# Kernel optimization log

Hardware: AMD Instinct MI355X
Metric: run time of the kernel (lower is better)

The kernel has to match this reference:

```python
import jax, jax.numpy as jnp
import numpy as np

N_NODES = 200_000
N_EDGES = 400_000
EMB_DIM = 128
HID_DIM = 24
N_TYPES = 8


def setup_inputs() -> dict:
    key = jax.random.key(0)
    k_emb, k_src, k_typ, k_w1, k_w2 = jax.random.split(key, 5)
    rgcn_emb = jax.random.normal(k_emb, (N_NODES, EMB_DIM), dtype=jnp.float32)
    edge_index = jax.random.randint(k_src, (2, N_EDGES), 0, N_NODES, dtype=jnp.int32)
    edge_type = jax.random.randint(k_typ, (N_EDGES,), 0, N_TYPES, dtype=jnp.int32)
    # per-edge-type 2-layer MLP params: Linear(2D->H), Linear(H->1)
    W1 = jax.random.normal(k_w1, (N_TYPES, 2 * EMB_DIM, HID_DIM), dtype=jnp.float32) * 0.05
    b1 = jnp.zeros((N_TYPES, HID_DIM), dtype=jnp.float32)
    W2 = jax.random.normal(k_w2, (N_TYPES, HID_DIM), dtype=jnp.float32) * 0.05
    b2 = jnp.zeros((N_TYPES,), dtype=jnp.float32)
    return {"rgcn_emb": rgcn_emb, "edge_index": edge_index, "edge_type": edge_type,
            "W1": W1, "b1": b1, "W2": W2, "b2": b2}


def reference(rgcn_emb, edge_index, edge_type, W1, b1, W2, b2):
    src, dst = edge_index[0], edge_index[1]
    # gather + concat: [E, 2D]
    edge_emb = jnp.concatenate([rgcn_emb[src], rgcn_emb[dst]], axis=-1)
    # dense per-type expert compute, then select by routing (MoE-style)
    h = jnp.einsum('ed,tdh->teh', edge_emb, W1) + b1[:, None, :]  # [T,E,H]
    h = jnp.where(h > 0, h, 0.01 * h)  # LeakyReLU(0.01)
    s = jnp.einsum('teh,th->te', h, W2) + b2[:, None]  # [T,E]
    onehot = jax.nn.one_hot(edge_type, N_TYPES, dtype=s.dtype)  # [E,T]
    scores = jnp.einsum('te,et->e', s, onehot)  # scatter-select per edge
    return (scores, rgcn_emb)
```

## Files before the change

### kernel.cpp

```cpp
#include <hip/hip_runtime.h>


typedef _Float16 h2 __attribute__((ext_vector_type(2)));
typedef float    f4 __attribute__((ext_vector_type(4)));

constexpr int N_NODES = 200000;
constexpr int N_EDGES = 400000;
constexpr int EMB_DIM = 128;
constexpr int HID     = 24;
constexpr int N_TYPES = 8;
constexpr int BLK     = 256;

constexpr int CHUNKS  = 128;
constexpr int CH_SZ   = N_EDGES / CHUNKS;
constexpr int MAX_PAD = N_EDGES + N_TYPES * (BLK - 1);
constexpr int SCORE_BLOCKS = (MAX_PAD + BLK - 1) / BLK;
constexpr int COPY_BLOCKS  = 1024;

constexpr int PREP_HIST = CHUNKS;
constexpr int PREP_W1   = 16;
constexpr int PREP_CONV = 1024;
constexpr int PREP_BLOCKS = PREP_HIST + PREP_W1 + PREP_CONV;

constexpr int OFF_CC     = 0;
constexpr int OFF_COUNTS = OFF_CC + CHUNKS * N_TYPES;
constexpr int OFF_POFF   = OFF_COUNTS + N_TYPES;
constexpr int OFF_SORTED = OFF_POFF + N_TYPES;
constexpr size_t SORT_BYTES  = (size_t)(OFF_SORTED + MAX_PAD) * sizeof(int);
constexpr size_t EMB16_OFF   = (SORT_BYTES + 255) & ~(size_t)255;
constexpr size_t EMB16_BYTES = (size_t)N_NODES * EMB_DIM * 2;
constexpr size_t W16_OFF     = EMB16_OFF + EMB16_BYTES;
constexpr size_t W16_BYTES   = (size_t)N_TYPES * 128 * HID * sizeof(int);
constexpr size_t NEED16      = W16_OFF + W16_BYTES;

__device__ __forceinline__ float fdot2f(h2 a, h2 b, float c) {
#if __has_builtin(__builtin_amdgcn_fdot2)
    return __builtin_amdgcn_fdot2(a, b, c, false);
#else
    return c + (float)a[0] * (float)b[0] + (float)a[1] * (float)b[1];
#endif
}

__global__ __launch_bounds__(BLK) void prep_k(
        const int* __restrict__ etype, int* __restrict__ ws,
        const float* __restrict__ emb, int2* __restrict__ emb16,
        const float* __restrict__ W1, h2* __restrict__ w16) {
    int b = blockIdx.x;
    if (b < PREP_HIST) {
        __shared__ int lc[N_TYPES];
        if (threadIdx.x < N_TYPES) lc[threadIdx.x] = 0;
        __syncthreads();
        int e0 = b * CH_SZ;
        for (int e = e0 + (int)threadIdx.x; e < e0 + CH_SZ; e += BLK)
            atomicAdd(&lc[etype[e]], 1);
        __syncthreads();
        if (threadIdx.x < N_TYPES)
            ws[OFF_CC + b * N_TYPES + threadIdx.x] = lc[threadIdx.x];
    } else if (b < PREP_HIST + PREP_W1) {
        int cb = b - PREP_HIST;
        for (int p = cb * BLK + threadIdx.x; p < N_TYPES * 128 * HID; p += PREP_W1 * BLK) {
            int t   = p / (128 * HID);
            int rem = p - t * 128 * HID;
            int kp  = rem / HID, j = rem - kp * HID;
            h2 v;
            v[0] = (_Float16)W1[(t * 256 + 2 * kp)     * HID + j];
            v[1] = (_Float16)W1[(t * 256 + 2 * kp + 1) * HID + j];
            w16[p] = v;
        }
    } else {
        int cb = b - PREP_HIST - PREP_W1;
        const f4* in4 = (const f4*)emb;
        const int n4 = N_NODES * EMB_DIM / 4;
        for (int i = cb * BLK + threadIdx.x; i < n4; i += PREP_CONV * BLK) {
            f4 a = in4[i];
            union { int2 v; h2 h[2]; } u;
            u.h[0] = h2{(_Float16)a.x, (_Float16)a.y};
            u.h[1] = h2{(_Float16)a.z, (_Float16)a.w};
            emb16[i] = u.v;
        }
    }
}

__global__ __launch_bounds__(BLK) void scatter_k(
        const int* __restrict__ etype, int* __restrict__ ws) {
    __shared__ int sbase[N_TYPES];
    __shared__ int tot[N_TYPES];
    __shared__ int mybase[N_TYPES];
    __shared__ int spoff[N_TYPES];
    __shared__ int lc[N_TYPES];
    int b = blockIdx.x;
    if (threadIdx.x < N_TYPES) {
        int t = threadIdx.x, s = 0, mb = 0;
        for (int c = 0; c < CHUNKS; ++c) {
            if (c == b) mb = s;
            s += ws[OFF_CC + c * N_TYPES + t];
        }
        tot[t] = s;
        mybase[t] = mb;
        lc[t] = 0;
    }
    __syncthreads();
    if (threadIdx.x == 0) {
        int off = 0;
        for (int t = 0; t < N_TYPES; ++t) {
            spoff[t] = off;
            off += ((tot[t] + BLK - 1) / BLK) * BLK;
        }
    }
    __syncthreads();
    if (threadIdx.x < N_TYPES) {
        sbase[threadIdx.x] = spoff[threadIdx.x] + mybase[threadIdx.x];
        if (b == 0) {
            ws[OFF_COUNTS + threadIdx.x] = tot[threadIdx.x];
            ws[OFF_POFF + threadIdx.x]   = spoff[threadIdx.x];
        }
    }
    __syncthreads();
    int e0 = b * CH_SZ;
    int* sorted = ws + OFF_SORTED;
    for (int e = e0 + (int)threadIdx.x; e < e0 + CH_SZ; e += BLK) {
        int t = etype[e];
        int r = atomicAdd(&lc[t], 1);
        sorted[sbase[t] + r] = e;
    }
}

__device__ __forceinline__ void do_copy(const float* __restrict__ emb,
                                        float* __restrict__ out, int cb, int nb) {
    const f4* s4 = (const f4*)emb;
    f4* o4 = (f4*)(out + N_EDGES);
    const int n4 = N_NODES * EMB_DIM / 4;
    for (int i = cb * BLK + (int)threadIdx.x; i < n4; i += nb * BLK) {
        f4 a = s4[i];
        __builtin_nontemporal_store(a, &o4[i]);
    }
}

__device__ __forceinline__ void compute_chunk(const int4* __restrict__ r,
                                              const h2* __restrict__ wrow,
                                              float acc[HID]) {
    const h2* hp = (const h2*)r;
#pragma unroll
    for (int kp = 0; kp < 32; ++kp) {
#pragma unroll
        for (int j = 0; j < HID; ++j)
            acc[j] = fdot2f(hp[kp], wrow[kp * HID + j], acc[j]);
    }
}

__global__ __launch_bounds__(BLK) void score16_k(
        const unsigned short* __restrict__ emb16u, const float* __restrict__ emb,
        const int* __restrict__ srci, const int* __restrict__ dsti,
        const int* __restrict__ ws,
        const h2* __restrict__ w16, const float* __restrict__ b1,
        const float* __restrict__ W2, const float* __restrict__ b2,
        float* __restrict__ out) {
    int b = blockIdx.x;
    if (b >= SCORE_BLOCKS) {
        do_copy(emb, out, b - SCORE_BLOCKS, (int)gridDim.x - SCORE_BLOCKS);
        return;
    }
    int poff[N_TYPES], counts[N_TYPES];
#pragma unroll
    for (int t = 0; t < N_TYPES; ++t) {
        counts[t] = ws[OFF_COUNTS + t];
        poff[t]   = ws[OFF_POFF + t];
    }
    int off = poff[N_TYPES - 1] + ((counts[N_TYPES - 1] + BLK - 1) / BLK) * BLK;
    int slot0 = b * BLK;
    if (slot0 >= off) return;
    int t = 0;
#pragma unroll
    for (int i = 1; i < N_TYPES; ++i)
        if (slot0 >= poff[i]) t = i;
    t = __builtin_amdgcn_readfirstlane(t);
    int cnt = counts[t];
    int local = slot0 - poff[t] + (int)threadIdx.x;
    if (local >= cnt) return;
    const int* sorted = ws + OFF_SORTED;
    int e = sorted[slot0 + threadIdx.x];
    int s = srci[e], d = dsti[e];

    float acc[HID];
#pragma unroll
    for (int j = 0; j < HID; ++j) acc[j] = b1[t * HID + j];
    const h2* wt = w16 + (size_t)t * 128 * HID;
    const int4* x0 = (const int4*)(emb16u + (size_t)s * EMB_DIM);
    const int4* x1 = (const int4*)(emb16u + (size_t)d * EMB_DIM);

    int4 A[8], B[8];
#pragma unroll
    for (int k = 0; k < 8; ++k) A[k] = x0[k];
#pragma unroll
    for (int k = 0; k < 8; ++k) B[k] = x0[8 + k];
    compute_chunk(A, wt + 0 * 32 * HID, acc);
#pragma unroll
    for (int k = 0; k < 8; ++k) A[k] = x1[k];
    compute_chunk(B, wt + 1 * 32 * HID, acc);
#pragma unroll
    for (int k = 0; k < 8; ++k) B[k] = x1[8 + k];
    compute_chunk(A, wt + 2 * 32 * HID, acc);
    compute_chunk(B, wt + 3 * 32 * HID, acc);

    float sc = b2[t];
#pragma unroll
    for (int j = 0; j < HID; ++j) {
        float h = acc[j];
        h = (h > 0.f) ? h : 0.01f * h;
        sc = fmaf(h, W2[t * HID + j], sc);
    }
    out[e] = sc;
}

__global__ __launch_bounds__(BLK) void fallback_k(
        const float* __restrict__ emb,
        const int* __restrict__ srci, const int* __restrict__ dsti,
        const int* __restrict__ etype,
        const float* __restrict__ W1, const float* __restrict__ b1,
        const float* __restrict__ W2, const float* __restrict__ b2,
        float* __restrict__ out) {
    long long i0 = (long long)blockIdx.x * BLK + threadIdx.x;
    const f4* s4 = (const f4*)emb;
    f4* o4 = (f4*)(out + N_EDGES);
    const long long n4 = (long long)N_NODES * EMB_DIM / 4;
    for (long long i = i0; i < n4; i += (long long)gridDim.x * BLK)
        o4[i] = s4[i];
    for (int e = (int)i0; e < N_EDGES; e += gridDim.x * BLK) {
        int t = etype[e];
        int s = srci[e], d = dsti[e];
        float acc[HID];
#pragma unroll
        for (int j = 0; j < HID; ++j) acc[j] = b1[t * HID + j];
        const float* w = W1 + (size_t)t * 2 * EMB_DIM * HID;
        for (int k = 0; k < EMB_DIM; ++k) {
            float x = emb[(size_t)s * EMB_DIM + k];
#pragma unroll
            for (int j = 0; j < HID; ++j) acc[j] = fmaf(x, w[k * HID + j], acc[j]);
        }
        for (int k = 0; k < EMB_DIM; ++k) {
            float x = emb[(size_t)d * EMB_DIM + k];
#pragma unroll
            for (int j = 0; j < HID; ++j) acc[j] = fmaf(x, w[(EMB_DIM + k) * HID + j], acc[j]);
        }
        float sc = b2[t];
#pragma unroll
        for (int j = 0; j < HID; ++j) {
            float h = acc[j];
            h = (h > 0.f) ? h : 0.01f * h;
            sc = fmaf(h, W2[t * HID + j], sc);
        }
        out[e] = sc;
    }
}

extern "C" void kernel_launch(void* const* d_in, const int* in_sizes, int n_in,
                              void* d_out, int out_size, void* d_ws, size_t ws_size,
                              hipStream_t stream) {
    const float* emb   = (const float*)d_in[0];
    const int*   eidx  = (const int*)d_in[1];
    const int*   etype = (const int*)d_in[2];
    const float* W1    = (const float*)d_in[3];
    const float* b1    = (const float*)d_in[4];
    const float* W2    = (const float*)d_in[5];
    const float* b2    = (const float*)d_in[6];
    float* out = (float*)d_out;
    const int* srci = eidx;
    const int* dsti = eidx + N_EDGES;

    if (ws_size >= NEED16) {
        int*  ws    = (int*)d_ws;
        int2* emb16 = (int2*)((char*)d_ws + EMB16_OFF);
        h2*   w16   = (h2*)((char*)d_ws + W16_OFF);
        prep_k<<<PREP_BLOCKS, BLK, 0, stream>>>(etype, ws, emb, emb16, W1, w16);
        scatter_k<<<CHUNKS, BLK, 0, stream>>>(etype, ws);
        score16_k<<<SCORE_BLOCKS + COPY_BLOCKS, BLK, 0, stream>>>(
            (const unsigned short*)emb16, emb, srci, dsti, ws,
            w16, b1, W2, b2, out);
    } else {
        fallback_k<<<2048, BLK, 0, stream>>>(emb, srci, dsti, etype, W1, b1, W2, b2, out);
    }
}
```

Measured before the change: 283.4 us.

## Drop fp16 embedding conversion pass and compute edge MLP directly in fp32

Removes the prep pass that converted the whole embedding table and W1 to fp16 every call, replacing it with a plain histogram kernel. The score kernel now gathers fp32 embedding rows directly and runs fp32 FMAs against W1 in chunks of float4 rows. This removes a full read-and-write pass over the table, in exchange for gathering twice as many bytes per edge and doing twice as many multiply-add instructions as packed fp16 dot2. The fallback path is also changed to reuse the vectorised fp32 helper.

After: 264.2 us. 6.8% less time.

```diff
diff --git a/kernel.cpp b/kernel.cpp
--- a/kernel.cpp
+++ b/kernel.cpp
@@ -1,8 +1,7 @@
 #include <hip/hip_runtime.h>
 
 
-typedef _Float16 h2 __attribute__((ext_vector_type(2)));
-typedef float    f4 __attribute__((ext_vector_type(4)));
+typedef float f4 __attribute__((ext_vector_type(4)));
 
 constexpr int N_NODES = 200000;
 constexpr int N_EDGES = 400000;
@@ -17,68 +16,26 @@
 constexpr int SCORE_BLOCKS = (MAX_PAD + BLK - 1) / BLK;
 constexpr int COPY_BLOCKS  = 1024;
 
-constexpr int PREP_HIST = CHUNKS;
-constexpr int PREP_W1   = 16;
-constexpr int PREP_CONV = 1024;
-constexpr int PREP_BLOCKS = PREP_HIST + PREP_W1 + PREP_CONV;
-
 constexpr int OFF_CC     = 0;
 constexpr int OFF_COUNTS = OFF_CC + CHUNKS * N_TYPES;
 constexpr int OFF_POFF   = OFF_COUNTS + N_TYPES;
 constexpr int OFF_SORTED = OFF_POFF + N_TYPES;
-constexpr size_t SORT_BYTES  = (size_t)(OFF_SORTED + MAX_PAD) * sizeof(int);
-constexpr size_t EMB16_OFF   = (SORT_BYTES + 255) & ~(size_t)255;
-constexpr size_t EMB16_BYTES = (size_t)N_NODES * EMB_DIM * 2;
-constexpr size_t W16_OFF     = EMB16_OFF + EMB16_BYTES;
-constexpr size_t W16_BYTES   = (size_t)N_TYPES * 128 * HID * sizeof(int);
-constexpr size_t NEED16      = W16_OFF + W16_BYTES;
-
-__device__ __forceinline__ float fdot2f(h2 a, h2 b, float c) {
-#if __has_builtin(__builtin_amdgcn_fdot2)
-    return __builtin_amdgcn_fdot2(a, b, c, false);
-#else
-    return c + (float)a[0] * (float)b[0] + (float)a[1] * (float)b[1];
-#endif
-}
-
-__global__ __launch_bounds__(BLK) void prep_k(
-        const int* __restrict__ etype, int* __restrict__ ws,
-        const float* __restrict__ emb, int2* __restrict__ emb16,
-        const float* __restrict__ W1, h2* __restrict__ w16) {
+constexpr size_t WS_NEED = (size_t)(OFF_SORTED + MAX_PAD) * sizeof(int);
+
+__global__ __launch_bounds__(BLK) void hist_k(const int* __restrict__ etype,
+                                              int* __restrict__ ws) {
+    __shared__ int lc[N_TYPES];
     int b = blockIdx.x;
-    if (b < PREP_HIST) {
-        __shared__ int lc[N_TYPES];
-        if (threadIdx.x < N_TYPES) lc[threadIdx.x] = 0;
-        __syncthreads();
-        int e0 = b * CH_SZ;
-        for (int e = e0 + (int)threadIdx.x; e < e0 + CH_SZ; e += BLK)
-            atomicAdd(&lc[etype[e]], 1);
-        __syncthreads();
-        if (threadIdx.x < N_TYPES)
-            ws[OFF_CC + b * N_TYPES + threadIdx.x] = lc[threadIdx.x];
-    } else if (b < PREP_HIST + PREP_W1) {
-        int cb = b - PREP_HIST;
-        for (int p = cb * BLK + threadIdx.x; p < N_TYPES * 128 * HID; p += PREP_W1 * BLK) {
-            int t   = p / (128 * HID);
-            int rem = p - t * 128 * HID;
-            int kp  = rem / HID, j = rem - kp * HID;
-            h2 v;
-            v[0] = (_Float16)W1[(t * 256 + 2 * kp)     * HID + j];
-            v[1] = (_Float16)W1[(t * 256 + 2 * kp + 1) * HID + j];
-            w16[p] = v;
-        }
-    } else {
-        int cb = b - PREP_HIST - PREP_W1;
-        const f4* in4 = (const f4*)emb;
-        const int n4 = N_NODES * EMB_DIM / 4;
-        for (int i = cb * BLK + threadIdx.x; i < n4; i += PREP_CONV * BLK) {
-            f4 a = in4[i];
-            union { int2 v; h2 h[2]; } u;
-            u.h[0] = h2{(_Float16)a.x, (_Float16)a.y};
-            u.h[1] = h2{(_Float16)a.z, (_Float16)a.w};
-            emb16[i] = u.v;
-        }
-    }
+    if (threadIdx.x < N_TYPES) lc[threadIdx.x] = 0;
+    __syncthreads();
+    int e0 = b * CH_SZ;
+    const int4* et4 = (const int4*)(etype + e0);
+    for (int e = e0 + (int)threadIdx.x; e < e0 + CH_SZ; e += BLK)
+        atomicAdd(&lc[etype[e]], 1);
+    (void)et4;
+    __syncthreads();
+    if (threadIdx.x < N_TYPES)
+        ws[OFF_CC + b * N_TYPES + threadIdx.x] = lc[threadIdx.x];
 }
 
 __global__ __launch_bounds__(BLK) void scatter_k(
@@ -136,23 +93,34 @@
     }
 }
 
-__device__ __forceinline__ void compute_chunk(const int4* __restrict__ r,
-                                              const h2* __restrict__ wrow,
-                                              float acc[HID]) {
-    const h2* hp = (const h2*)r;
-#pragma unroll
-    for (int kp = 0; kp < 32; ++kp) {
-#pragma unroll
-        for (int j = 0; j < HID; ++j)
-            acc[j] = fdot2f(hp[kp], wrow[kp * HID + j], acc[j]);
-    }
-}
-
-__global__ __launch_bounds__(BLK) void score16_k(
-        const unsigned short* __restrict__ emb16u, const float* __restrict__ emb,
+__device__ __forceinline__ void half_mm(const f4* __restrict__ x4,
+                                        const float* __restrict__ w,
+                                        float acc[HID]) {
+#pragma unroll 1
+    for (int c = 0; c < 4; ++c) {
+        f4 r[8];
+#pragma unroll
+        for (int k = 0; k < 8; ++k) r[k] = x4[c * 8 + k];
+#pragma unroll
+        for (int k = 0; k < 8; ++k) {
+            const float* wp = w + (c * 32 + k * 4) * HID;
+#pragma unroll
+            for (int j = 0; j < HID; ++j) acc[j] = fmaf(r[k][0], wp[0 * HID + j], acc[j]);
+#pragma unroll
+            for (int j = 0; j < HID; ++j) acc[j] = fmaf(r[k][1], wp[1 * HID + j], acc[j]);
+#pragma unroll
+            for (int j = 0; j < HID; ++j) acc[j] = fmaf(r[k][2], wp[2 * HID + j], acc[j]);
+#pragma unroll
+            for (int j = 0; j < HID; ++j) acc[j] = fmaf(r[k][3], wp[3 * HID + j], acc[j]);
+        }
+    }
+}
+
+__global__ __launch_bounds__(BLK) void score32_k(
+        const float* __restrict__ emb,
         const int* __restrict__ srci, const int* __restrict__ dsti,
         const int* __restrict__ ws,
-        const h2* __restrict__ w16, const float* __restrict__ b1,
+        const float* __restrict__ W1, const float* __restrict__ b1,
         const float* __restrict__ W2, const float* __restrict__ b2,
         float* __restrict__ out) {
     int b = blockIdx.x;
@@ -184,24 +152,9 @@
     float acc[HID];
 #pragma unroll
     for (int j = 0; j < HID; ++j) acc[j] = b1[t * HID + j];
-    const h2* wt = w16 + (size_t)t * 128 * HID;
-    const int4* x0 = (const int4*)(emb16u + (size_t)s * EMB_DIM);
-    const int4* x1 = (const int4*)(emb16u + (size_t)d * EMB_DIM);
-
-    int4 A[8], B[8];
-#pragma unroll
-    for (int k = 0; k < 8; ++k) A[k] = x0[k];
-#pragma unroll
-    for (int k = 0; k < 8; ++k) B[k] = x0[8 + k];
-    compute_chunk(A, wt + 0 * 32 * HID, acc);
-#pragma unroll
-    for (int k = 0; k < 8; ++k) A[k] = x1[k];
-    compute_chunk(B, wt + 1 * 32 * HID, acc);
-#pragma unroll
-    for (int k = 0; k < 8; ++k) B[k] = x1[8 + k];
-    compute_chunk(A, wt + 2 * 32 * HID, acc);
-    compute_chunk(B, wt + 3 * 32 * HID, acc);
-
+    const float* W1t = W1 + (size_t)t * (2 * EMB_DIM * HID);
+    half_mm((const f4*)(emb + (size_t)s * EMB_DIM), W1t, acc);
+    half_mm((const f4*)(emb + (size_t)d * EMB_DIM), W1t + EMB_DIM * HID, acc);
     float sc = b2[t];
 #pragma unroll
     for (int j = 0; j < HID; ++j) {
@@ -232,16 +185,8 @@
 #pragma unroll
         for (int j = 0; j < HID; ++j) acc[j] = b1[t * HID + j];
         const float* w = W1 + (size_t)t * 2 * EMB_DIM * HID;
-        for (int k = 0; k < EMB_DIM; ++k) {
-            float x = emb[(size_t)s * EMB_DIM + k];
-#pragma unroll
-            for (int j = 0; j < HID; ++j) acc[j] = fmaf(x, w[k * HID + j], acc[j]);
-        }
-        for (int k = 0; k < EMB_DIM; ++k) {
-            float x = emb[(size_t)d * EMB_DIM + k];
-#pragma unroll
-            for (int j = 0; j < HID; ++j) acc[j] = fmaf(x, w[(EMB_DIM + k) * HID + j], acc[j]);
-        }
+        half_mm((const f4*)(emb + (size_t)s * EMB_DIM), w, acc);
+        half_mm((const f4*)(emb + (size_t)d * EMB_DIM), w + EMB_DIM * HID, acc);
         float sc = b2[t];
 #pragma unroll
         for (int j = 0; j < HID; ++j) {
@@ -267,15 +212,12 @@
     const int* srci = eidx;
     const int* dsti = eidx + N_EDGES;
 
-    if (ws_size >= NEED16) {
-        int*  ws    = (int*)d_ws;
-        int2* emb16 = (int2*)((char*)d_ws + EMB16_OFF);
-        h2*   w16   = (h2*)((char*)d_ws + W16_OFF);
-        prep_k<<<PREP_BLOCKS, BLK, 0, stream>>>(etype, ws, emb, emb16, W1, w16);
+    if (ws_size >= WS_NEED) {
+        int* ws = (int*)d_ws;
+        hist_k<<<CHUNKS, BLK, 0, stream>>>(etype, ws);
         scatter_k<<<CHUNKS, BLK, 0, stream>>>(etype, ws);
-        score16_k<<<SCORE_BLOCKS + COPY_BLOCKS, BLK, 0, stream>>>(
-            (const unsigned short*)emb16, emb, srci, dsti, ws,
-            w16, b1, W2, b2, out);
+        score32_k<<<SCORE_BLOCKS + COPY_BLOCKS, BLK, 0, stream>>>(
+            emb, srci, dsti, ws, W1, b1, W2, b2, out);
     } else {
         fallback_k<<<2048, BLK, 0, stream>>>(emb, srci, dsti, etype, W1, b1, W2, b2, out);
     }
```
